# Kernel tuning notes

Measured on AMD Instinct MI355X. Metric: run time of the kernel, lower is better.

## Reference

```python
import jax, jax.numpy as jnp
import numpy as np

HIDDEN = 512
LATENT = 256
NUM_NODE_TYPES = 16


def setup_inputs() -> dict:
    key = jax.random.key(0)
    ks = jax.random.split(key, 9)
    s = lambda fan_in: 1.0 / np.sqrt(fan_in)
    return {
        "z": jax.random.normal(ks[0], (1024, LATENT), dtype=jnp.float32),
        "num_nodes": 128,
        "W_z": jax.random.uniform(ks[1], (LATENT, HIDDEN), jnp.float32, -s(LATENT), s(LATENT)),
        "b_z": jax.random.uniform(ks[2], (HIDDEN,), jnp.float32, -s(LATENT), s(LATENT)),
        "W_node": jax.random.uniform(ks[3], (HIDDEN, NUM_NODE_TYPES), jnp.float32, -s(HIDDEN), s(HIDDEN)),
        "b_node": jax.random.uniform(ks[4], (NUM_NODE_TYPES,), jnp.float32, -s(HIDDEN), s(HIDDEN)),
        "W_e1": jax.random.uniform(ks[5], (2 * HIDDEN, HIDDEN), jnp.float32, -s(2 * HIDDEN), s(2 * HIDDEN)),
        "b_e1": jax.random.uniform(ks[6], (HIDDEN,), jnp.float32, -s(2 * HIDDEN), s(2 * HIDDEN)),
        "W_e2": jax.random.uniform(ks[7], (HIDDEN, 1), jnp.float32, -s(HIDDEN), s(HIDDEN)),
        "b_e2": jax.random.uniform(ks[8], (1,), jnp.float32, -s(HIDDEN), s(HIDDEN)),
    }


def reference(z, num_nodes, W_z, b_z, W_node, b_node, W_e1, b_e1, W_e2, b_e2):
    # h: [B, H]
    h = jax.nn.relu(z @ W_z + b_z)
    B = z.shape[0]
    # h_expanded: [B, N, H] (same h replicated per node, as in the original)
    h_expanded = jnp.broadcast_to(h[:, None, :], (B, num_nodes, h.shape[-1]))
    node_logits = h_expanded @ W_node + b_node  # [B, N, T]
    # Every (i, j) pair in the original loop uses cat(h, h) -> identical scalar per batch.
    h_pair = jnp.concatenate([h, h], axis=-1)  # [B, 2H]
    p = jax.nn.sigmoid(jax.nn.relu(h_pair @ W_e1 + b_e1) @ W_e2 + b_e2)  # [B, 1]
    # Scatter onto strict lower triangle (j < i), zeros elsewhere.
    tril = jnp.tril(jnp.ones((num_nodes, num_nodes), dtype=z.dtype), k=-1)  # [N, N]
    edge_probs = p[:, :, None] * tril[None, :, :]  # [B, N, N]
    return node_logits, edge_probs
```

## Files before the change

kernel.cpp:

```cpp
#include <hip/hip_runtime.h>
#include <hip/hip_bf16.h>
#include <math.h>

#define BB 1024
#define LL 256
#define HH 512
#define TT 16
#define NN 128

#define NODE_F4 (BB * NN * TT / 4)
#define EDGE_F4 (BB * NN * NN / 4)

typedef short bf16x8 __attribute__((ext_vector_type(8)));
typedef short s16x4  __attribute__((ext_vector_type(4)));
typedef float f32x4  __attribute__((ext_vector_type(4)));

static __device__ __forceinline__ short bfbits(float f) {
    __hip_bfloat16 h = __float2bfloat16(f);
    return *reinterpret_cast<short*>(&h);
}

__device__ __forceinline__ void transpose_tile(const float* __restrict__ in,
                                               __hip_bfloat16* __restrict__ out,
                                               int k0, int n0, int Kdim, bool fold,
                                               __hip_bfloat16 (*tile)[34]) {
    const int tx = threadIdx.x & 31;
    const int ty = threadIdx.x >> 5;
    #pragma unroll
    for (int r = ty; r < 32; r += 8) {
        float v = in[(k0 + r) * HH + n0 + tx];
        if (fold) v += in[(k0 + r + HH) * HH + n0 + tx];
        tile[r][tx] = __float2bfloat16(v);
    }
    __syncthreads();
    #pragma unroll
    for (int r = ty; r < 32; r += 8) {
        out[(n0 + r) * Kdim + k0 + tx] = tile[tx][r];
    }
}

__global__ __launch_bounds__(256) void k_prep(const float* __restrict__ z,
                                              const float* __restrict__ Wz,
                                              const float* __restrict__ We1,
                                              const float* __restrict__ Wn,
                                              __hip_bfloat16* __restrict__ z_bf,
                                              __hip_bfloat16* __restrict__ WzT,
                                              __hip_bfloat16* __restrict__ WsumT,
                                              __hip_bfloat16* __restrict__ WnT,
                                              float* __restrict__ p_acc) {
    __shared__ __hip_bfloat16 tile[32][34];
    const int bid = blockIdx.x;
    const int tid = threadIdx.x;
    if (bid < 256) {
        const int q = bid * 256 + tid;
        float4 v = ((const float4*)z)[q];
        s16x4 o; o.x = bfbits(v.x); o.y = bfbits(v.y); o.z = bfbits(v.z); o.w = bfbits(v.w);
        ((s16x4*)z_bf)[q] = o;
    } else if (bid < 384) {
        const int t = bid - 256;
        transpose_tile(Wz, WzT, (t >> 4) * 32, (t & 15) * 32, LL, false, tile);
    } else if (bid < 640) {
        const int t = bid - 384;
        transpose_tile(We1, WsumT, (t >> 4) * 32, (t & 15) * 32, HH, true, tile);
    } else if (bid < 672) {
        const int u = (bid - 640) * 256 + tid;
        const int tt = u >> 9, k = u & 511;
        WnT[u] = __float2bfloat16(Wn[k * TT + tt]);
    } else {
        ((float4*)p_acc)[tid] = make_float4(0.f, 0.f, 0.f, 0.f);
    }
}

__global__ __launch_bounds__(256) void k_gemm1(const __hip_bfloat16* __restrict__ A,
                                               const __hip_bfloat16* __restrict__ Bt,
                                               const float* __restrict__ bias,
                                               __hip_bfloat16* __restrict__ out) {
    const int wid  = (blockIdx.x << 2) + (threadIdx.x >> 6);
    const int lane = threadIdx.x & 63;
    const int mt = wid >> 5, nt = wid & 31;
    const int l16 = lane & 15, quad = lane >> 4;

    const short* Ap = (const short*)A  + (mt * 16 + l16) * LL + quad * 8;
    const short* Bp = (const short*)Bt + (nt * 16 + l16) * LL + quad * 8;

    f32x4 acc = {0.f, 0.f, 0.f, 0.f};
    #pragma unroll
    for (int kt = 0; kt < LL / 32; ++kt) {
        bf16x8 a = *(const bf16x8*)(Ap + kt * 32);
        bf16x8 b = *(const bf16x8*)(Bp + kt * 32);
        acc = __builtin_amdgcn_mfma_f32_16x16x32_bf16(a, b, acc, 0, 0, 0);
    }
    const int col = nt * 16 + l16;
    const float bb = bias[col];
    #pragma unroll
    for (int r = 0; r < 4; ++r) {
        out[(mt * 16 + quad * 4 + r) * HH + col] = __float2bfloat16(fmaxf(acc[r] + bb, 0.f));
    }
}

__global__ __launch_bounds__(256) void k_gemm2_phead(const __hip_bfloat16* __restrict__ A,
                                                     const __hip_bfloat16* __restrict__ Bt,
                                                     const float* __restrict__ be1,
                                                     const float* __restrict__ We2,
                                                     float* __restrict__ p_acc) {
    const int wid  = (blockIdx.x << 2) + (threadIdx.x >> 6);
    const int lane = threadIdx.x & 63;
    const int mt = wid >> 5, nt = wid & 31;
    const int l16 = lane & 15, quad = lane >> 4;

    const short* Ap = (const short*)A  + (mt * 16 + l16) * HH + quad * 8;
    const short* Bp = (const short*)Bt + (nt * 16 + l16) * HH + quad * 8;

    f32x4 acc = {0.f, 0.f, 0.f, 0.f};
    #pragma unroll
    for (int kt = 0; kt < HH / 32; ++kt) {
        bf16x8 a = *(const bf16x8*)(Ap + kt * 32);
        bf16x8 b = *(const bf16x8*)(Bp + kt * 32);
        acc = __builtin_amdgcn_mfma_f32_16x16x32_bf16(a, b, acc, 0, 0, 0);
    }
    const int col = nt * 16 + l16;
    const float bb = be1[col];
    const float w2 = We2[col];
    float sr[4];
    #pragma unroll
    for (int r = 0; r < 4; ++r) sr[r] = fmaxf(acc[r] + bb, 0.f) * w2;
    #pragma unroll
    for (int off = 1; off < 16; off <<= 1) {
        #pragma unroll
        for (int r = 0; r < 4; ++r) sr[r] += __shfl_xor(sr[r], off);
    }
    if (l16 == 0) {
        #pragma unroll
        for (int r = 0; r < 4; ++r)
            atomicAdd(p_acc + mt * 16 + quad * 4 + r, sr[r]);
    }
}

__global__ __launch_bounds__(256) void k_small(const __hip_bfloat16* __restrict__ h,
                                               const __hip_bfloat16* __restrict__ WnT,
                                               const float* __restrict__ bn,
                                               const float* __restrict__ p_acc,
                                               const float* __restrict__ be2,
                                               float* __restrict__ node16,
                                               float* __restrict__ p) {
    const int wid  = (blockIdx.x << 2) + (threadIdx.x >> 6);
    const int lane = threadIdx.x & 63;
    const int l16 = lane & 15, quad = lane >> 4;

    const short* Ap = (const short*)h   + (wid * 16 + l16) * HH + quad * 8;
    const short* Bp = (const short*)WnT + l16 * HH + quad * 8;

    f32x4 acc = {0.f, 0.f, 0.f, 0.f};
    #pragma unroll
    for (int kt = 0; kt < HH / 32; ++kt) {
        bf16x8 a = *(const bf16x8*)(Ap + kt * 32);
        bf16x8 b = *(const bf16x8*)(Bp + kt * 32);
        acc = __builtin_amdgcn_mfma_f32_16x16x32_bf16(a, b, acc, 0, 0, 0);
    }
    const float bb = bn[l16];
    #pragma unroll
    for (int r = 0; r < 4; ++r)
        node16[(wid * 16 + quad * 4 + r) * TT + l16] = acc[r] + bb;

    const int idx = blockIdx.x * 256 + threadIdx.x;
    if (idx < BB) {
        float t = p_acc[idx] + be2[0];
        p[idx] = 1.f / (1.f + expf(-t));
    }
}

__global__ __launch_bounds__(256) void k_write(const float* __restrict__ node16,
                                               const float* __restrict__ p,
                                               float4* __restrict__ out) {
    const int q = blockIdx.x * 256 + threadIdx.x;
    if (q < NODE_F4) {
        const int b  = q >> 9;
        const int t4 = q & 3;
        out[q] = ((const float4*)(node16 + b * TT))[t4];
    } else {
        const int e  = q - NODE_F4;
        const int b  = e >> 12;
        const int i  = (e >> 5) & 127;
        const int j0 = (e & 31) * 4;
        const float pv = p[b];
        float4 v;
        v.x = (j0 + 0 < i) ? pv : 0.f;
        v.y = (j0 + 1 < i) ? pv : 0.f;
        v.z = (j0 + 2 < i) ? pv : 0.f;
        v.w = (j0 + 3 < i) ? pv : 0.f;
        out[q] = v;
    }
}

extern "C" void kernel_launch(void* const* d_in, const int* in_sizes, int n_in,
                              void* d_out, int out_size, void* d_ws, size_t ws_size,
                              hipStream_t stream) {
    const float* z    = (const float*)d_in[0];
    const float* Wz   = (const float*)d_in[2];
    const float* bz   = (const float*)d_in[3];
    const float* Wn   = (const float*)d_in[4];
    const float* bn   = (const float*)d_in[5];
    const float* We1  = (const float*)d_in[6];
    const float* be1  = (const float*)d_in[7];
    const float* We2  = (const float*)d_in[8];
    const float* be2  = (const float*)d_in[9];
    float* out = (float*)d_out;

    char* base = (char*)d_ws;
    __hip_bfloat16* z_bf   = (__hip_bfloat16*)(base);
    __hip_bfloat16* WzT    = (__hip_bfloat16*)(base +  512 * 1024);
    __hip_bfloat16* WsumT  = (__hip_bfloat16*)(base +  768 * 1024);
    __hip_bfloat16* WnT    = (__hip_bfloat16*)(base + 1280 * 1024);
    __hip_bfloat16* h_bf   = (__hip_bfloat16*)(base + 1296 * 1024);
    float*          node16 = (float*)(base + 2320 * 1024);
    float*          p_acc  = (float*)(base + 2384 * 1024);
    float*          p      = (float*)(base + 2388 * 1024);

    k_prep<<<673, 256, 0, stream>>>(z, Wz, We1, Wn, z_bf, WzT, WsumT, WnT, p_acc);

    k_gemm1<<<512, 256, 0, stream>>>(z_bf, WzT, bz, h_bf);

    k_gemm2_phead<<<512, 256, 0, stream>>>(h_bf, WsumT, be1, We2, p_acc);

    k_small<<<16, 256, 0, stream>>>(h_bf, WnT, bn, p_acc, be2, node16, p);

    k_write<<<(NODE_F4 + EDGE_F4) / 256, 256, 0, stream>>>(node16, p, (float4*)out);

    (void)in_sizes; (void)n_in; (void)out_size; (void)ws_size;
}
```

Baseline: 127.4 us.

## Fuse both GEMMs, node head and edge head into one per-row-block kernel

Replaces the separate gemm1, gemm2+p-head and small-head kernels with a single 1024-thread kernel per 16-row block. It converts z to bf16 in shared memory, keeps h in LDS, and reduces the edge-head partials in shared memory instead of with global atomics. This removes two launches, the h_bf global round trip and the p_acc zeroing. The cost is only 64 blocks on a GPU with many more CUs, so each block streams the full weight matrices itself and parallelism drops sharply.

```diff
diff --git a/kernel.cpp b/kernel.cpp
--- a/kernel.cpp
+++ b/kernel.cpp
@@ -39,133 +39,141 @@
     }
 }
 
-__global__ __launch_bounds__(256) void k_prep(const float* __restrict__ z,
-                                              const float* __restrict__ Wz,
+__global__ __launch_bounds__(256) void k_prep(const float* __restrict__ Wz,
                                               const float* __restrict__ We1,
                                               const float* __restrict__ Wn,
-                                              __hip_bfloat16* __restrict__ z_bf,
                                               __hip_bfloat16* __restrict__ WzT,
                                               __hip_bfloat16* __restrict__ WsumT,
-                                              __hip_bfloat16* __restrict__ WnT,
-                                              float* __restrict__ p_acc) {
+                                              __hip_bfloat16* __restrict__ WnT) {
     __shared__ __hip_bfloat16 tile[32][34];
     const int bid = blockIdx.x;
-    const int tid = threadIdx.x;
-    if (bid < 256) {
-        const int q = bid * 256 + tid;
-        float4 v = ((const float4*)z)[q];
-        s16x4 o; o.x = bfbits(v.x); o.y = bfbits(v.y); o.z = bfbits(v.z); o.w = bfbits(v.w);
-        ((s16x4*)z_bf)[q] = o;
+    if (bid < 128) {
+        const int t = bid;
+        transpose_tile(Wz, WzT, (t >> 4) * 32, (t & 15) * 32, LL, false, tile);
     } else if (bid < 384) {
-        const int t = bid - 256;
-        transpose_tile(Wz, WzT, (t >> 4) * 32, (t & 15) * 32, LL, false, tile);
-    } else if (bid < 640) {
-        const int t = bid - 384;
+        const int t = bid - 128;
         transpose_tile(We1, WsumT, (t >> 4) * 32, (t & 15) * 32, HH, true, tile);
-    } else if (bid < 672) {
-        const int u = (bid - 640) * 256 + tid;
-        const int tt = u >> 9, k = u & 511;
-        WnT[u] = __float2bfloat16(Wn[k * TT + tt]);
     } else {
-        ((float4*)p_acc)[tid] = make_float4(0.f, 0.f, 0.f, 0.f);
-    }
-}
-
-__global__ __launch_bounds__(256) void k_gemm1(const __hip_bfloat16* __restrict__ A,
-                                               const __hip_bfloat16* __restrict__ Bt,
-                                               const float* __restrict__ bias,
-                                               __hip_bfloat16* __restrict__ out) {
-    const int wid  = (blockIdx.x << 2) + (threadIdx.x >> 6);
-    const int lane = threadIdx.x & 63;
-    const int mt = wid >> 5, nt = wid & 31;
-    const int l16 = lane & 15, quad = lane >> 4;
-
-    const short* Ap = (const short*)A  + (mt * 16 + l16) * LL + quad * 8;
-    const short* Bp = (const short*)Bt + (nt * 16 + l16) * LL + quad * 8;
-
-    f32x4 acc = {0.f, 0.f, 0.f, 0.f};
-    #pragma unroll
-    for (int kt = 0; kt < LL / 32; ++kt) {
-        bf16x8 a = *(const bf16x8*)(Ap + kt * 32);
-        bf16x8 b = *(const bf16x8*)(Bp + kt * 32);
-        acc = __builtin_amdgcn_mfma_f32_16x16x32_bf16(a, b, acc, 0, 0, 0);
-    }
-    const int col = nt * 16 + l16;
-    const float bb = bias[col];
-    #pragma unroll
-    for (int r = 0; r < 4; ++r) {
-        out[(mt * 16 + quad * 4 + r) * HH + col] = __float2bfloat16(fmaxf(acc[r] + bb, 0.f));
-    }
-}
-
-__global__ __launch_bounds__(256) void k_gemm2_phead(const __hip_bfloat16* __restrict__ A,
-                                                     const __hip_bfloat16* __restrict__ Bt,
-                                                     const float* __restrict__ be1,
-                                                     const float* __restrict__ We2,
-                                                     float* __restrict__ p_acc) {
-    const int wid  = (blockIdx.x << 2) + (threadIdx.x >> 6);
-    const int lane = threadIdx.x & 63;
-    const int mt = wid >> 5, nt = wid & 31;
-    const int l16 = lane & 15, quad = lane >> 4;
-
-    const short* Ap = (const short*)A  + (mt * 16 + l16) * HH + quad * 8;
-    const short* Bp = (const short*)Bt + (nt * 16 + l16) * HH + quad * 8;
-
-    f32x4 acc = {0.f, 0.f, 0.f, 0.f};
-    #pragma unroll
-    for (int kt = 0; kt < HH / 32; ++kt) {
-        bf16x8 a = *(const bf16x8*)(Ap + kt * 32);
-        bf16x8 b = *(const bf16x8*)(Bp + kt * 32);
-        acc = __builtin_amdgcn_mfma_f32_16x16x32_bf16(a, b, acc, 0, 0, 0);
-    }
-    const int col = nt * 16 + l16;
-    const float bb = be1[col];
-    const float w2 = We2[col];
-    float sr[4];
-    #pragma unroll
-    for (int r = 0; r < 4; ++r) sr[r] = fmaxf(acc[r] + bb, 0.f) * w2;
-    #pragma unroll
-    for (int off = 1; off < 16; off <<= 1) {
-        #pragma unroll
-        for (int r = 0; r < 4; ++r) sr[r] += __shfl_xor(sr[r], off);
-    }
-    if (l16 == 0) {
+        const int u = (bid - 384) * 256 + threadIdx.x;
+        WnT[u] = __float2bfloat16(Wn[(u & 511) * TT + (u >> 9)]);
+    }
+}
+
+__global__ __launch_bounds__(1024) void k_fused(const float* __restrict__ z,
+                                                const __hip_bfloat16* __restrict__ WzT,
+                                                const __hip_bfloat16* __restrict__ WsumT,
+                                                const __hip_bfloat16* __restrict__ WnT,
+                                                const float* __restrict__ bz,
+                                                const float* __restrict__ be1,
+                                                const float* __restrict__ We2,
+                                                const float* __restrict__ be2,
+                                                const float* __restrict__ bn,
+                                                float* __restrict__ node16,
+                                                float* __restrict__ p) {
+    constexpr int ZP = 264;
+    constexpr int HP = 520;
+    __shared__ short z_s[16 * ZP];
+    __shared__ short h_s[16 * HP];
+    __shared__ float red[16][16];
+    __shared__ float nacc[16][256];
+
+    const int tid  = threadIdx.x;
+    const int w    = tid >> 6;
+    const int lane = tid & 63;
+    const int l16  = lane & 15;
+    const int quad = lane >> 4;
+    const int row0 = blockIdx.x * 16;
+
+    {
+        float4 v = ((const float4*)(z + row0 * LL))[tid];
+        const int r = tid >> 6;
+        const int c = (tid & 63) * 4;
+        s16x4 o;
+        o.x = bfbits(v.x); o.y = bfbits(v.y); o.z = bfbits(v.z); o.w = bfbits(v.w);
+        *(s16x4*)(z_s + r * ZP + c) = o;
+    }
+    __syncthreads();
+
+    const int nt0 = 2 * w, nt1 = 2 * w + 1;
+    const int c0 = nt0 * 16 + l16, c1 = nt1 * 16 + l16;
+
+    f32x4 a0 = {0.f, 0.f, 0.f, 0.f}, a1 = {0.f, 0.f, 0.f, 0.f};
+    {
+        const short* Az = z_s + l16 * ZP + quad * 8;
+        const short* B0 = (const short*)WzT + c0 * LL + quad * 8;
+        const short* B1 = (const short*)WzT + c1 * LL + quad * 8;
+        #pragma unroll 4
+        for (int kt = 0; kt < LL / 32; ++kt) {
+            bf16x8 a  = *(const bf16x8*)(Az + kt * 32);
+            bf16x8 b0 = *(const bf16x8*)(B0 + kt * 32);
+            bf16x8 b1 = *(const bf16x8*)(B1 + kt * 32);
+            a0 = __builtin_amdgcn_mfma_f32_16x16x32_bf16(a, b0, a0, 0, 0, 0);
+            a1 = __builtin_amdgcn_mfma_f32_16x16x32_bf16(a, b1, a1, 0, 0, 0);
+        }
+    }
+    {
+        const float bb0 = bz[c0], bb1 = bz[c1];
+        #pragma unroll
+        for (int r = 0; r < 4; ++r) {
+            h_s[(quad * 4 + r) * HP + c0] = bfbits(fmaxf(a0[r] + bb0, 0.f));
+            h_s[(quad * 4 + r) * HP + c1] = bfbits(fmaxf(a1[r] + bb1, 0.f));
+        }
+    }
+    __syncthreads();
+
+    a0 = (f32x4){0.f, 0.f, 0.f, 0.f}; a1 = (f32x4){0.f, 0.f, 0.f, 0.f};
+    {
+        const short* Ah = h_s + l16 * HP + quad * 8;
+        const short* B0 = (const short*)WsumT + c0 * HH + quad * 8;
+        const short* B1 = (const short*)WsumT + c1 * HH + quad * 8;
+        #pragma unroll 4
+        for (int kt = 0; kt < HH / 32; ++kt) {
+            bf16x8 a  = *(const bf16x8*)(Ah + kt * 32);
+            bf16x8 b0 = *(const bf16x8*)(B0 + kt * 32);
+            bf16x8 b1 = *(const bf16x8*)(B1 + kt * 32);
+            a0 = __builtin_amdgcn_mfma_f32_16x16x32_bf16(a, b0, a0, 0, 0, 0);
+            a1 = __builtin_amdgcn_mfma_f32_16x16x32_bf16(a, b1, a1, 0, 0, 0);
+        }
+    }
+    {
+        const float e0 = be1[c0], e1b = be1[c1];
+        const float w0 = We2[c0], w1 = We2[c1];
+        float s[4];
         #pragma unroll
         for (int r = 0; r < 4; ++r)
-            atomicAdd(p_acc + mt * 16 + quad * 4 + r, sr[r]);
-    }
-}
-
-__global__ __launch_bounds__(256) void k_small(const __hip_bfloat16* __restrict__ h,
-                                               const __hip_bfloat16* __restrict__ WnT,
-                                               const float* __restrict__ bn,
-                                               const float* __restrict__ p_acc,
-                                               const float* __restrict__ be2,
-                                               float* __restrict__ node16,
-                                               float* __restrict__ p) {
-    const int wid  = (blockIdx.x << 2) + (threadIdx.x >> 6);
-    const int lane = threadIdx.x & 63;
-    const int l16 = lane & 15, quad = lane >> 4;
-
-    const short* Ap = (const short*)h   + (wid * 16 + l16) * HH + quad * 8;
-    const short* Bp = (const short*)WnT + l16 * HH + quad * 8;
-
-    f32x4 acc = {0.f, 0.f, 0.f, 0.f};
-    #pragma unroll
-    for (int kt = 0; kt < HH / 32; ++kt) {
-        bf16x8 a = *(const bf16x8*)(Ap + kt * 32);
-        bf16x8 b = *(const bf16x8*)(Bp + kt * 32);
-        acc = __builtin_amdgcn_mfma_f32_16x16x32_bf16(a, b, acc, 0, 0, 0);
-    }
-    const float bb = bn[l16];
-    #pragma unroll
-    for (int r = 0; r < 4; ++r)
-        node16[(wid * 16 + quad * 4 + r) * TT + l16] = acc[r] + bb;
-
-    const int idx = blockIdx.x * 256 + threadIdx.x;
-    if (idx < BB) {
-        float t = p_acc[idx] + be2[0];
-        p[idx] = 1.f / (1.f + expf(-t));
+            s[r] = fmaxf(a0[r] + e0, 0.f) * w0 + fmaxf(a1[r] + e1b, 0.f) * w1;
+        #pragma unroll
+        for (int off = 1; off < 16; off <<= 1) {
+            #pragma unroll
+            for (int r = 0; r < 4; ++r) s[r] += __shfl_xor(s[r], off);
+        }
+        if (l16 == 0) {
+            #pragma unroll
+            for (int r = 0; r < 4; ++r) red[w][quad * 4 + r] = s[r];
+        }
+    }
+
+    {
+        bf16x8 a = *(const bf16x8*)(h_s + l16 * HP + w * 32 + quad * 8);
+        bf16x8 b = *(const bf16x8*)((const short*)WnT + l16 * HH + w * 32 + quad * 8);
+        f32x4 na = {0.f, 0.f, 0.f, 0.f};
+        na = __builtin_amdgcn_mfma_f32_16x16x32_bf16(a, b, na, 0, 0, 0);
+        #pragma unroll
+        for (int r = 0; r < 4; ++r) nacc[w][(quad * 4 + r) * 16 + l16] = na[r];
+    }
+    __syncthreads();
+
+    if (tid < 16) {
+        float s = be2[0];
+        #pragma unroll
+        for (int ww = 0; ww < 16; ++ww) s += red[ww][tid];
+        p[row0 + tid] = 1.f / (1.f + expf(-s));
+    }
+    if (tid < 256) {
+        float s = bn[tid & 15];
+        #pragma unroll
+        for (int ww = 0; ww < 16; ++ww) s += nacc[ww][tid];
+        node16[(row0 + (tid >> 4)) * TT + (tid & 15)] = s;
     }
 }
 
@@ -207,22 +215,16 @@
     float* out = (float*)d_out;
 
     char* base = (char*)d_ws;
-    __hip_bfloat16* z_bf   = (__hip_bfloat16*)(base);
-    __hip_bfloat16* WzT    = (__hip_bfloat16*)(base +  512 * 1024);
-    __hip_bfloat16* WsumT  = (__hip_bfloat16*)(base +  768 * 1024);
-    __hip_bfloat16* WnT    = (__hip_bfloat16*)(base + 1280 * 1024);
-    __hip_bfloat16* h_bf   = (__hip_bfloat16*)(base + 1296 * 1024);
-    float*          node16 = (float*)(base + 2320 * 1024);
-    float*          p_acc  = (float*)(base + 2384 * 1024);
-    float*          p      = (float*)(base + 2388 * 1024);
-
-    k_prep<<<673, 256, 0, stream>>>(z, Wz, We1, Wn, z_bf, WzT, WsumT, WnT, p_acc);
-
-    k_gemm1<<<512, 256, 0, stream>>>(z_bf, WzT, bz, h_bf);
-
-    k_gemm2_phead<<<512, 256, 0, stream>>>(h_bf, WsumT, be1, We2, p_acc);
-
-    k_small<<<16, 256, 0, stream>>>(h_bf, WnT, bn, p_acc, be2, node16, p);
+    __hip_bfloat16* WzT    = (__hip_bfloat16*)(base);
+    __hip_bfloat16* WsumT  = (__hip_bfloat16*)(base +  256 * 1024);
+    __hip_bfloat16* WnT    = (__hip_bfloat16*)(base +  768 * 1024);
+    float*          node16 = (float*)(base + 784 * 1024);
+    float*          p      = (float*)(base + 848 * 1024);
+
+    k_prep<<<416, 256, 0, stream>>>(Wz, We1, Wn, WzT, WsumT, WnT);
+
+    k_fused<<<64, 1024, 0, stream>>>(z, WzT, WsumT, WnT, bz, be1, We2, be2, bn,
+                                     node16, p);
 
     k_write<<<(NODE_F4 + EDGE_F4) / 256, 256, 0, stream>>>(node16, p, (float4*)out);
 
```

New measurement: 129.9 us. About the same (+1.9%).
